# Kernel tuning notes

Measured on AMD Instinct MI355X. Metric: run time of the kernel, lower is better.

The kernel has to match this reference:

```python
import jax, jax.numpy as jnp
import numpy as np

IOU_THRESHOLD = 0.5
CLASS_CONF_THRESHOLD = 0.01
MAX_OUTPUT = 100  # tf.image.non_max_suppression max_output_size


def _nms_indices(boxes, scores, max_out, iou_thr):
    """Fixed-size greedy NMS: returns (idxs[max_out], valid[max_out])."""
    x1, y1, x2, y2 = boxes[:, 0], boxes[:, 1], boxes[:, 2], boxes[:, 3]
    areas = (x2 - x1) * (y2 - y1)

    def body(sc, _):
        i = jnp.argmax(sc)
        valid = sc[i] > 0.0  # score_threshold = 0.0 in tf call
        xx1 = jnp.maximum(x1[i], x1)
        yy1 = jnp.maximum(y1[i], y1)
        xx2 = jnp.minimum(x2[i], x2)
        yy2 = jnp.minimum(y2[i], y2)
        inter = jnp.maximum(xx2 - xx1, 0.0) * jnp.maximum(yy2 - yy1, 0.0)
        union = areas[i] + areas - inter
        iou = jnp.where(union > 0.0, inter / union, 0.0)
        # suppress overlapping boxes (self included, iou=1) only if pick valid
        sc_new = jnp.where((iou > iou_thr) & valid, -1.0, sc)
        return sc_new, (i, valid)

    _, (idxs, valids) = jax.lax.scan(body, scores, None, length=max_out)
    return idxs, valids


def _decode(x, anchors):
    B, H, W, A, C = x.shape  # B == 1
    gw = jnp.float32(W)
    # grid offsets: (col, row) per cell, matching cell_x / transposed cell_y
    cx = jnp.broadcast_to(jnp.arange(W, dtype=jnp.float32).reshape(1, 1, W, 1, 1), (1, H, W, 1, 1))
    cy = jnp.broadcast_to(jnp.arange(H, dtype=jnp.float32).reshape(1, H, 1, 1, 1), (1, H, W, 1, 1))
    grid = jnp.concatenate([cx, cy], axis=-1)  # (1,H,W,1,2)

    xy = (jax.nn.sigmoid(x[..., 0:2]) + grid) / gw                      # (B,H,W,A,2)
    wh = jnp.exp(x[..., 2:4]) * anchors.reshape(1, 1, 1, A, 2) / gw     # (B,H,W,A,2)
    boxes = jnp.concatenate([xy - wh / 2.0, xy + wh / 2.0], axis=-1)    # (B,H,W,A,4)

    conf = jax.nn.sigmoid(x[..., 4:5])                                  # (B,H,W,A,1)
    cls_prob = jax.nn.softmax(x[..., 5:], axis=-1)                      # (B,H,W,A,C-5)
    class_confidence = conf * cls_prob
    masked = jnp.where(class_confidence > CLASS_CONF_THRESHOLD, class_confidence, 0.0)
    classes = jnp.argmax(masked, axis=-1).astype(jnp.int32)             # (B,H,W,A)
    confm = jnp.max(masked, axis=-1)                                    # (B,H,W,A)

    N = H * W * A
    return boxes.reshape(N, 4), confm.reshape(N), classes.reshape(N)


def reference(x, anchors):
    boxes, scores, classes = _decode(x, anchors)
    idxs, valids = _nms_indices(jax.lax.stop_gradient(boxes),
                                jax.lax.stop_gradient(scores),
                                MAX_OUTPUT, IOU_THRESHOLD)
    sel_conf = jnp.where(valids, scores[idxs], 0.0)
    sel_boxes = jnp.where(valids[:, None], boxes[idxs], 0.0)
    sel_classes = jnp.where(valids, classes[idxs], -1)
    return sel_conf, sel_boxes, sel_classes


def setup_inputs() -> dict:
    key = jax.random.key(0)
    k1, k2 = jax.random.split(key)
    x = jax.random.normal(k1, (1, 256, 256, 5, 85), dtype=jnp.float32)
    # anchor priors in grid units (positive widths/heights)
    anchors = jax.random.uniform(k2, (5, 2), dtype=jnp.float32) * 4.0 + 0.5
    return {"x": x, "anchors": anchors}
```

## Files before the change

### kernel.cpp

```cpp
#include <hip/hip_runtime.h>
#include <hip/hip_bf16.h>

#define NROW 327680
#define NCLS 80
#define K_TARGET 1024u
#define CAP 2048u
#define MAX_OUT 100
#define NBIN 864
#define BIN0 0x3C23
#define HIST_BLOCKS 80

#define WS_SCORES 0
#define WS_PART   1310720
#define WS_CNT    1587200
#define WS_KEYS   1587264

typedef float f4v __attribute__((ext_vector_type(4)));
typedef f4v f4u __attribute__((aligned(4)));

__global__ __launch_bounds__(256, 1) void decode_score(
    const float* __restrict__ x, float* __restrict__ scores) {
  const int r = blockIdx.x * 256 + threadIdx.x;
  const float* rp = x + (size_t)r * 85;

  float conf_l = rp[4];
  float cl[80];
  #pragma unroll
  for (int c = 0; c < 20; ++c) {
    f4v t4 = *(const f4u*)(rp + 5 + 4 * c);
    cl[4*c+0] = t4.x; cl[4*c+1] = t4.y; cl[4*c+2] = t4.z; cl[4*c+3] = t4.w;
  }

  float m = cl[0];
  #pragma unroll
  for (int c = 1; c < NCLS; ++c) { float l = cl[c]; if (l > m) m = l; }
  float s = 0.f;
  #pragma unroll
  for (int c = 0; c < NCLS; ++c) s += expf(cl[c] - m);
  float conf = 1.f / (1.f + expf(-conf_l));
  float best = conf * (1.f / s);
  scores[r] = (best > 0.01f) ? best : 0.f;
}

__global__ __launch_bounds__(1024) void hist_kernel(
    const float* __restrict__ scores, unsigned* __restrict__ part) {
  __shared__ unsigned h[NBIN];
  const int t = threadIdx.x;
  if (t < NBIN) h[t] = 0;
  __syncthreads();

  float4 s4 = ((const float4*)scores)[blockIdx.x * 1024 + t];
  float sv[4] = {s4.x, s4.y, s4.z, s4.w};
  #pragma unroll
  for (int k = 0; k < 4; ++k) {
    float s = sv[k];
    if (s > 0.f) {
      int idx = (int)(__float_as_uint(s) >> 16) - BIN0;
      if (idx > NBIN - 1) idx = NBIN - 1;
      atomicAdd(&h[idx], 1u);
    }
  }
  __syncthreads();
  if (t < NBIN) part[blockIdx.x * NBIN + t] = h[t];
}

__global__ __launch_bounds__(1024) void thresh_kernel(
    const unsigned* __restrict__ part, unsigned* __restrict__ cnt) {
  __shared__ unsigned bufA[1024], bufB[1024];
  const int t = threadIdx.x;

  unsigned colsum = 0;
  if (t < NBIN) {
    unsigned a0 = 0, a1 = 0, a2 = 0, a3 = 0;
    #pragma unroll
    for (int b = 0; b < HIST_BLOCKS; b += 4) {
      a0 += part[(b + 0) * NBIN + t];
      a1 += part[(b + 1) * NBIN + t];
      a2 += part[(b + 2) * NBIN + t];
      a3 += part[(b + 3) * NBIN + t];
    }
    colsum = a0 + a1 + a2 + a3;
  }
  bufA[t] = colsum;
  __syncthreads();

  unsigned* src = bufA; unsigned* dst = bufB;
  for (int d = 1; d < 1024; d <<= 1) {
    unsigned val = src[t] + ((t + d < 1024) ? src[t + d] : 0u);
    dst[t] = val;
    __syncthreads();
    unsigned* tmp = src; src = dst; dst = tmp;
  }
  if (src[t] >= K_TARGET && (t == 1023 || src[t + 1] < K_TARGET)) {
    unsigned T = (unsigned)t;
    if (src[t] > CAP) T += 1;
    cnt[1] = T;
  }
  if (t == 0) {
    if (src[0] < K_TARGET) cnt[1] = 0;
    cnt[0] = 0;
  }
}

__global__ __launch_bounds__(256) void compact_kernel(
    const float* __restrict__ scores, unsigned* __restrict__ cnt,
    unsigned long long* __restrict__ keys) {
  __shared__ unsigned blocal, bbase;
  const int t = threadIdx.x;
  if (t == 0) blocal = 0;
  __syncthreads();

  const unsigned T = cnt[1];
  const int gi = blockIdx.x * 256 + t;
  float4 s4 = ((const float4*)scores)[gi];
  float sv[4] = {s4.x, s4.y, s4.z, s4.w};
  unsigned long long lk[4]; int nl = 0;
  #pragma unroll
  for (int k = 0; k < 4; ++k) {
    float s = sv[k];
    if (s <= 0.f) continue;
    unsigned bits = __float_as_uint(s);
    int idx = (int)(bits >> 16) - BIN0;
    if (idx > NBIN - 1) idx = NBIN - 1;
    if ((unsigned)idx < T) continue;
    unsigned r = (unsigned)(gi * 4 + k);
    lk[nl++] = ((unsigned long long)bits << 32) |
               (unsigned long long)(0xFFFFFFFFu - r);
  }
  unsigned lpos = nl ? atomicAdd(&blocal, (unsigned)nl) : 0u;
  __syncthreads();
  if (t == 0 && blocal) bbase = atomicAdd(&cnt[0], blocal);
  __syncthreads();
  if (nl) {
    unsigned base = bbase + lpos;
    for (int i = 0; i < nl; ++i)
      if (base + i < CAP) keys[base + i] = lk[i];
  }
}

__global__ __launch_bounds__(1024) void final_kernel(
    const float* __restrict__ x, const float* __restrict__ anchors,
    const unsigned* __restrict__ cnt, const unsigned long long* __restrict__ keys,
    float* __restrict__ out) {
  __shared__ unsigned long long sk[CAP];
  __shared__ float4 cbox[CAP];
  __shared__ float4 kbox[MAX_OUT];
  __shared__ float  kscore[MAX_OUT];
  __shared__ int    krow[MAX_OUT];
  __shared__ int    kcls[MAX_OUT];
  __shared__ int    knum;
  const int t = threadIdx.x;
  if (t == 0) knum = 0;

  unsigned n = cnt[0]; if (n > CAP) n = CAP;
  unsigned npow2 = 2; while (npow2 < n) npow2 <<= 1;
  for (unsigned i = t; i < npow2; i += 1024) sk[i] = (i < n) ? keys[i] : 0ull;
  __syncthreads();

  for (unsigned k = 2; k <= npow2; k <<= 1) {
    for (unsigned j = k >> 1; j > 0; j >>= 1) {
      for (unsigned p = t; p < (npow2 >> 1); p += 1024) {
        unsigned i = ((p & ~(j - 1u)) << 1) | (p & (j - 1u));
        unsigned ixj = i | j;
        unsigned long long a = sk[i], b = sk[ixj];
        bool desc = ((i & k) == 0);
        if (desc ? (a < b) : (a > b)) { sk[i] = b; sk[ixj] = a; }
      }
      __syncthreads();
    }
  }

  for (unsigned i = t; i < n; i += 1024) {
    unsigned r = 0xFFFFFFFFu - (unsigned)(sk[i] & 0xFFFFFFFFull);
    const float* rp = x + (size_t)r * 85;
    float tx = rp[0], ty = rp[1], tw = rp[2], th = rp[3];
    const int a  = (int)(r % 5u);
    const int hw = (int)(r / 5u);
    const float wf = (float)(hw & 255);
    const float hf = (float)(hw >> 8);
    float sx = 1.f / (1.f + expf(-tx));
    float sy = 1.f / (1.f + expf(-ty));
    float xc = (sx + wf) / 256.f;
    float yc = (sy + hf) / 256.f;
    float bw = expf(tw) * anchors[2*a]     / 256.f;
    float bh = expf(th) * anchors[2*a + 1] / 256.f;
    float hwd = bw / 2.f, hhd = bh / 2.f;
    cbox[i] = make_float4(xc - hwd, yc - hhd, xc + hwd, yc + hhd);
  }
  __syncthreads();

  if (t < 64) {
    int nk = 0;
    float ax1=0,ay1=0,ax2=0,ay2=0,aar=0;
    float bx1=0,by1=0,bx2=0,by2=0,bar=0;
    unsigned long long key = (n > 0) ? sk[0] : 0ull;
    float4 bb = (n > 0) ? cbox[0] : make_float4(0,0,0,0);
    for (unsigned cc = 0; cc < n && nk < MAX_OUT; ++cc) {
      unsigned long long key_n = (cc + 1 < n) ? sk[cc + 1] : 0ull;
      float4 bb_n = (cc + 1 < n) ? cbox[cc + 1] : make_float4(0,0,0,0);
      unsigned sbits = (unsigned)(key >> 32);
      if (sbits == 0u) break;
      float area = (bb.z - bb.x) * (bb.w - bb.y);
      bool s0 = false, s1 = false;
      if (t < nk) {
        float xx1 = fmaxf(ax1, bb.x), yy1 = fmaxf(ay1, bb.y);
        float xx2 = fminf(ax2, bb.z), yy2 = fminf(ay2, bb.w);
        float inter = fmaxf(xx2 - xx1, 0.f) * fmaxf(yy2 - yy1, 0.f);
        float uni = aar + area - inter;
        s0 = (uni > 0.f) && (inter / uni > 0.5f);
      }
      if (t + 64 < nk) {
        float xx1 = fmaxf(bx1, bb.x), yy1 = fmaxf(by1, bb.y);
        float xx2 = fminf(bx2, bb.z), yy2 = fminf(by2, bb.w);
        float inter = fmaxf(xx2 - xx1, 0.f) * fmaxf(yy2 - yy1, 0.f);
        float uni = bar + area - inter;
        s1 = (uni > 0.f) && (inter / uni > 0.5f);
      }
      if (!__any(s0 || s1)) {
        if (t == nk)      { ax1=bb.x; ay1=bb.y; ax2=bb.z; ay2=bb.w; aar=area; }
        if (t == nk - 64) { bx1=bb.x; by1=bb.y; bx2=bb.z; by2=bb.w; bar=area; }
        if (t == 0) {
          unsigned r = 0xFFFFFFFFu - (unsigned)(key & 0xFFFFFFFFull);
          kbox[nk] = bb; kscore[nk] = __uint_as_float(sbits); krow[nk] = (int)r;
        }
        ++nk;
      }
      key = key_n; bb = bb_n;
    }
    if (t == 0) knum = nk;
  }
  __syncthreads();

  {
    const int wv = t >> 6, lane = t & 63;
    for (int kidx = wv; kidx < knum; kidx += 16) {
      const float* rp = x + (size_t)krow[kidx] * 85;
      float l0 = rp[5 + lane];
      unsigned b0 = __float_as_uint(l0);
      b0 = (b0 & 0x80000000u) ? ~b0 : (b0 | 0x80000000u);
      unsigned long long kv =
          ((unsigned long long)b0 << 32) | (unsigned long long)(0xFFFFFFFFu - lane);
      if (lane < 16) {
        float l1 = rp[5 + 64 + lane];
        unsigned b1 = __float_as_uint(l1);
        b1 = (b1 & 0x80000000u) ? ~b1 : (b1 | 0x80000000u);
        unsigned long long kv1 =
            ((unsigned long long)b1 << 32) |
            (unsigned long long)(0xFFFFFFFFu - (64 + lane));
        if (kv1 > kv) kv = kv1;
      }
      #pragma unroll
      for (int d = 32; d >= 1; d >>= 1) {
        unsigned long long o = __shfl_xor((long long)kv, d, 64);
        if (o > kv) kv = o;
      }
      if (lane == 0)
        kcls[kidx] = (int)(0xFFFFFFFFu - (unsigned)(kv & 0xFFFFFFFFull));
    }
  }
  __syncthreads();

  if (t < MAX_OUT) {
    float conf = 0.f; float4 bb = make_float4(0.f, 0.f, 0.f, 0.f); float cf = -1.f;
    if (t < knum) { conf = kscore[t]; bb = kbox[t]; cf = (float)kcls[t]; }
    out[t] = conf;
    ((float4*)(out + 100))[t] = bb;
    out[500 + t] = cf;
  }
}

extern "C" void kernel_launch(void* const* d_in, const int* in_sizes, int n_in,
                              void* d_out, int out_size, void* d_ws, size_t ws_size,
                              hipStream_t stream) {
  const float* x       = (const float*)d_in[0];
  const float* anchors = (const float*)d_in[1];
  float* out = (float*)d_out;
  char* ws = (char*)d_ws;

  float*              scores = (float*)(ws + WS_SCORES);
  unsigned*           part   = (unsigned*)(ws + WS_PART);
  unsigned*           cnt    = (unsigned*)(ws + WS_CNT);
  unsigned long long* keys   = (unsigned long long*)(ws + WS_KEYS);

  hipLaunchKernelGGL(decode_score, dim3(NROW / 256), dim3(256),
                     0, stream, x, scores);
  hipLaunchKernelGGL(hist_kernel, dim3(HIST_BLOCKS), dim3(1024),
                     0, stream, scores, part);
  hipLaunchKernelGGL(thresh_kernel, dim3(1), dim3(1024), 0, stream, part, cnt);
  hipLaunchKernelGGL(compact_kernel, dim3(NROW / 1024), dim3(256),
                     0, stream, scores, cnt, keys);
  hipLaunchKernelGGL(final_kernel, dim3(1), dim3(1024), 0, stream,
                     x, anchors, cnt, keys, out);
}
```

Measured before the change: 237.8 us.

## Replace single-block bitonic sort and serial NMS with rank sort and IoU bitmask

The single-block bitonic sort is replaced by a multi-block rank-counting sort that also decodes candidate boxes. A new kernel precomputes a full pairwise IoU suppression bitmask matrix across many blocks. The greedy NMS loop then only ORs bitmask rows, with the first rows cached in LDS and later rows prefetched. This moves serial sort and IoU work off one workgroup, at the cost of two extra launches and the O(n^2) adjacency computation and its global writes.

```diff
diff --git a/kernel.cpp b/kernel.cpp
--- a/kernel.cpp
+++ b/kernel.cpp
@@ -5,18 +5,25 @@
 #define NCLS 80
 #define K_TARGET 1024u
 #define CAP 2048u
+#define MAXN 2048
 #define MAX_OUT 100
 #define NBIN 864
 #define BIN0 0x3C23
 #define HIST_BLOCKS 80
+#define ADJW 32
+#define ADJC_ROWS 128
 
 #define WS_SCORES 0
 #define WS_PART   1310720
 #define WS_CNT    1587200
 #define WS_KEYS   1587264
+#define WS_SORT   1603648
+#define WS_CBOX   1620032
+#define WS_ADJ    1652800
 
 typedef float f4v __attribute__((ext_vector_type(4)));
 typedef f4v f4u __attribute__((aligned(4)));
+typedef unsigned long long ull;
 
 __global__ __launch_bounds__(256, 1) void decode_score(
     const float* __restrict__ x, float* __restrict__ scores) {
@@ -104,7 +111,7 @@
 
 __global__ __launch_bounds__(256) void compact_kernel(
     const float* __restrict__ scores, unsigned* __restrict__ cnt,
-    unsigned long long* __restrict__ keys) {
+    ull* __restrict__ keys) {
   __shared__ unsigned blocal, bbase;
   const int t = threadIdx.x;
   if (t == 0) blocal = 0;
@@ -114,7 +121,7 @@
   const int gi = blockIdx.x * 256 + t;
   float4 s4 = ((const float4*)scores)[gi];
   float sv[4] = {s4.x, s4.y, s4.z, s4.w};
-  unsigned long long lk[4]; int nl = 0;
+  ull lk[4]; int nl = 0;
   #pragma unroll
   for (int k = 0; k < 4; ++k) {
     float s = sv[k];
@@ -124,8 +131,7 @@
     if (idx > NBIN - 1) idx = NBIN - 1;
     if ((unsigned)idx < T) continue;
     unsigned r = (unsigned)(gi * 4 + k);
-    lk[nl++] = ((unsigned long long)bits << 32) |
-               (unsigned long long)(0xFFFFFFFFu - r);
+    lk[nl++] = ((ull)bits << 32) | (ull)(0xFFFFFFFFu - r);
   }
   unsigned lpos = nl ? atomicAdd(&blocal, (unsigned)nl) : 0u;
   __syncthreads();
@@ -138,120 +144,141 @@
   }
 }
 
+__global__ __launch_bounds__(64) void rank_kernel(
+    const float* __restrict__ x, const float* __restrict__ anchors,
+    const unsigned* __restrict__ cnt, const ull* __restrict__ keys,
+    ull* __restrict__ sorted, float4* __restrict__ cboxg) {
+  __shared__ ull lk[MAXN];
+  unsigned n = cnt[0]; if (n > CAP) n = CAP;
+  const int t = threadIdx.x;
+  for (unsigned i = t; i < n; i += 64) lk[i] = keys[i];
+  __syncthreads();
+
+  const unsigned i = blockIdx.x * 64 + t;
+  if (i >= n) return;
+  const ull ki = lk[i];
+  unsigned rank = 0;
+  #pragma unroll 4
+  for (unsigned j = 0; j < n; ++j) rank += (lk[j] > ki) ? 1u : 0u;
+
+  sorted[rank] = ki;
+
+  unsigned r = 0xFFFFFFFFu - (unsigned)(ki & 0xFFFFFFFFull);
+  const float* rp = x + (size_t)r * 85;
+  float tx = rp[0], ty = rp[1], tw = rp[2], th = rp[3];
+  const int a  = (int)(r % 5u);
+  const int hw = (int)(r / 5u);
+  const float wf = (float)(hw & 255);
+  const float hf = (float)(hw >> 8);
+  float sx = 1.f / (1.f + expf(-tx));
+  float sy = 1.f / (1.f + expf(-ty));
+  float xc = (sx + wf) / 256.f;
+  float yc = (sy + hf) / 256.f;
+  float bw = expf(tw) * anchors[2*a]     / 256.f;
+  float bh = expf(th) * anchors[2*a + 1] / 256.f;
+  float hwd = bw / 2.f, hhd = bh / 2.f;
+  cboxg[rank] = make_float4(xc - hwd, yc - hhd, xc + hwd, yc + hhd);
+}
+
+__global__ __launch_bounds__(256) void adj_kernel(
+    const unsigned* __restrict__ cnt, const float4* __restrict__ cboxg,
+    ull* __restrict__ adj) {
+  unsigned n = cnt[0]; if (n > CAP) n = CAP;
+  const unsigned i = blockIdx.x;
+  if (i >= n) return;
+  const float4 bi = cboxg[i];
+  const float areai = (bi.z - bi.x) * (bi.w - bi.y);
+  const int t = threadIdx.x, wid = t >> 6, lane = t & 63;
+
+  #pragma unroll
+  for (int pass = 0; pass < 8; ++pass) {
+    unsigned j = (unsigned)(pass * 256 + t);
+    bool sup = false;
+    if (j < n) {
+      float4 bj = cboxg[j];
+      float xx1 = fmaxf(bi.x, bj.x), yy1 = fmaxf(bi.y, bj.y);
+      float xx2 = fminf(bi.z, bj.z), yy2 = fminf(bi.w, bj.w);
+      float inter = fmaxf(xx2 - xx1, 0.f) * fmaxf(yy2 - yy1, 0.f);
+      float areaj = (bj.z - bj.x) * (bj.w - bj.y);
+      float uni = areai + areaj - inter;
+      float iou = (uni > 0.f) ? (inter / uni) : 0.f;
+      sup = iou > 0.5f;
+    }
+    ull m = __ballot(sup);
+    if (lane == 0) adj[(size_t)i * ADJW + pass * 4 + wid] = m;
+  }
+}
+
 __global__ __launch_bounds__(1024) void final_kernel(
-    const float* __restrict__ x, const float* __restrict__ anchors,
-    const unsigned* __restrict__ cnt, const unsigned long long* __restrict__ keys,
-    float* __restrict__ out) {
-  __shared__ unsigned long long sk[CAP];
-  __shared__ float4 cbox[CAP];
-  __shared__ float4 kbox[MAX_OUT];
-  __shared__ float  kscore[MAX_OUT];
-  __shared__ int    krow[MAX_OUT];
-  __shared__ int    kcls[MAX_OUT];
-  __shared__ int    knum;
+    const float* __restrict__ x, const unsigned* __restrict__ cnt,
+    const ull* __restrict__ sorted, const float4* __restrict__ cboxg,
+    const ull* __restrict__ adjg, float* __restrict__ out) {
+  __shared__ ull sk[MAXN];
+  __shared__ ull adjc[ADJC_ROWS * ADJW];
+  __shared__ int keptcc[MAX_OUT];
+  __shared__ int kcls[MAX_OUT];
+  __shared__ int knum;
   const int t = threadIdx.x;
   if (t == 0) knum = 0;
 
   unsigned n = cnt[0]; if (n > CAP) n = CAP;
-  unsigned npow2 = 2; while (npow2 < n) npow2 <<= 1;
-  for (unsigned i = t; i < npow2; i += 1024) sk[i] = (i < n) ? keys[i] : 0ull;
-  __syncthreads();
-
-  for (unsigned k = 2; k <= npow2; k <<= 1) {
-    for (unsigned j = k >> 1; j > 0; j >>= 1) {
-      for (unsigned p = t; p < (npow2 >> 1); p += 1024) {
-        unsigned i = ((p & ~(j - 1u)) << 1) | (p & (j - 1u));
-        unsigned ixj = i | j;
-        unsigned long long a = sk[i], b = sk[ixj];
-        bool desc = ((i & k) == 0);
-        if (desc ? (a < b) : (a > b)) { sk[i] = b; sk[ixj] = a; }
+  for (unsigned i = t; i < n; i += 1024) sk[i] = sorted[i];
+  const unsigned ncache = (n < ADJC_ROWS ? n : ADJC_ROWS) * ADJW;
+  for (unsigned i = t; i < ncache; i += 1024) adjc[i] = adjg[i];
+  __syncthreads();
+
+  if (t < 64) {
+    const int lane = t;
+    ull mask = 0ull;
+    int nk = 0;
+    ull rA = 0ull, rB = 0ull;
+    if (lane < ADJW) {
+      if (n > 0) rA = adjc[0 * ADJW + lane];
+      if (n > 1) rB = (1 < ADJC_ROWS) ? adjc[1 * ADJW + lane]
+                                      : adjg[1 * ADJW + lane];
+    }
+    for (unsigned cc = 0; cc < n; ++cc) {
+      ull rC = 0ull;
+      unsigned pcc = cc + 2;
+      if (lane < ADJW && pcc < n)
+        rC = (pcc < ADJC_ROWS) ? adjc[pcc * ADJW + lane]
+                               : adjg[(size_t)pcc * ADJW + lane];
+      const int w = (int)(cc >> 6);
+      ull mw = (ull)__shfl((long long)mask, w, 64);
+      bool sup = (mw >> (cc & 63u)) & 1ull;
+      if (!sup) {
+        mask |= rA;
+        if (lane == 0) keptcc[nk] = (int)cc;
+        ++nk;
+        if (nk == MAX_OUT) break;
       }
-      __syncthreads();
-    }
-  }
-
-  for (unsigned i = t; i < n; i += 1024) {
-    unsigned r = 0xFFFFFFFFu - (unsigned)(sk[i] & 0xFFFFFFFFull);
-    const float* rp = x + (size_t)r * 85;
-    float tx = rp[0], ty = rp[1], tw = rp[2], th = rp[3];
-    const int a  = (int)(r % 5u);
-    const int hw = (int)(r / 5u);
-    const float wf = (float)(hw & 255);
-    const float hf = (float)(hw >> 8);
-    float sx = 1.f / (1.f + expf(-tx));
-    float sy = 1.f / (1.f + expf(-ty));
-    float xc = (sx + wf) / 256.f;
-    float yc = (sy + hf) / 256.f;
-    float bw = expf(tw) * anchors[2*a]     / 256.f;
-    float bh = expf(th) * anchors[2*a + 1] / 256.f;
-    float hwd = bw / 2.f, hhd = bh / 2.f;
-    cbox[i] = make_float4(xc - hwd, yc - hhd, xc + hwd, yc + hhd);
-  }
-  __syncthreads();
-
-  if (t < 64) {
-    int nk = 0;
-    float ax1=0,ay1=0,ax2=0,ay2=0,aar=0;
-    float bx1=0,by1=0,bx2=0,by2=0,bar=0;
-    unsigned long long key = (n > 0) ? sk[0] : 0ull;
-    float4 bb = (n > 0) ? cbox[0] : make_float4(0,0,0,0);
-    for (unsigned cc = 0; cc < n && nk < MAX_OUT; ++cc) {
-      unsigned long long key_n = (cc + 1 < n) ? sk[cc + 1] : 0ull;
-      float4 bb_n = (cc + 1 < n) ? cbox[cc + 1] : make_float4(0,0,0,0);
-      unsigned sbits = (unsigned)(key >> 32);
-      if (sbits == 0u) break;
-      float area = (bb.z - bb.x) * (bb.w - bb.y);
-      bool s0 = false, s1 = false;
-      if (t < nk) {
-        float xx1 = fmaxf(ax1, bb.x), yy1 = fmaxf(ay1, bb.y);
-        float xx2 = fminf(ax2, bb.z), yy2 = fminf(ay2, bb.w);
-        float inter = fmaxf(xx2 - xx1, 0.f) * fmaxf(yy2 - yy1, 0.f);
-        float uni = aar + area - inter;
-        s0 = (uni > 0.f) && (inter / uni > 0.5f);
-      }
-      if (t + 64 < nk) {
-        float xx1 = fmaxf(bx1, bb.x), yy1 = fmaxf(by1, bb.y);
-        float xx2 = fminf(bx2, bb.z), yy2 = fminf(by2, bb.w);
-        float inter = fmaxf(xx2 - xx1, 0.f) * fmaxf(yy2 - yy1, 0.f);
-        float uni = bar + area - inter;
-        s1 = (uni > 0.f) && (inter / uni > 0.5f);
-      }
-      if (!__any(s0 || s1)) {
-        if (t == nk)      { ax1=bb.x; ay1=bb.y; ax2=bb.z; ay2=bb.w; aar=area; }
-        if (t == nk - 64) { bx1=bb.x; by1=bb.y; bx2=bb.z; by2=bb.w; bar=area; }
-        if (t == 0) {
-          unsigned r = 0xFFFFFFFFu - (unsigned)(key & 0xFFFFFFFFull);
-          kbox[nk] = bb; kscore[nk] = __uint_as_float(sbits); krow[nk] = (int)r;
-        }
-        ++nk;
-      }
-      key = key_n; bb = bb_n;
-    }
-    if (t == 0) knum = nk;
-  }
-  __syncthreads();
+      rA = rB; rB = rC;
+    }
+    if (lane == 0) knum = nk;
+  }
+  __syncthreads();
+  const int kn = knum;
 
   {
     const int wv = t >> 6, lane = t & 63;
-    for (int kidx = wv; kidx < knum; kidx += 16) {
-      const float* rp = x + (size_t)krow[kidx] * 85;
+    for (int kidx = wv; kidx < kn; kidx += 16) {
+      ull key = sk[keptcc[kidx]];
+      unsigned r = 0xFFFFFFFFu - (unsigned)(key & 0xFFFFFFFFull);
+      const float* rp = x + (size_t)r * 85;
       float l0 = rp[5 + lane];
       unsigned b0 = __float_as_uint(l0);
       b0 = (b0 & 0x80000000u) ? ~b0 : (b0 | 0x80000000u);
-      unsigned long long kv =
-          ((unsigned long long)b0 << 32) | (unsigned long long)(0xFFFFFFFFu - lane);
+      ull kv = ((ull)b0 << 32) | (ull)(0xFFFFFFFFu - lane);
       if (lane < 16) {
         float l1 = rp[5 + 64 + lane];
         unsigned b1 = __float_as_uint(l1);
         b1 = (b1 & 0x80000000u) ? ~b1 : (b1 | 0x80000000u);
-        unsigned long long kv1 =
-            ((unsigned long long)b1 << 32) |
-            (unsigned long long)(0xFFFFFFFFu - (64 + lane));
+        ull kv1 = ((ull)b1 << 32) | (ull)(0xFFFFFFFFu - (64 + lane));
         if (kv1 > kv) kv = kv1;
       }
       #pragma unroll
       for (int d = 32; d >= 1; d >>= 1) {
-        unsigned long long o = __shfl_xor((long long)kv, d, 64);
+        ull o = (ull)__shfl_xor((long long)kv, d, 64);
         if (o > kv) kv = o;
       }
       if (lane == 0)
@@ -262,7 +289,13 @@
 
   if (t < MAX_OUT) {
     float conf = 0.f; float4 bb = make_float4(0.f, 0.f, 0.f, 0.f); float cf = -1.f;
-    if (t < knum) { conf = kscore[t]; bb = kbox[t]; cf = (float)kcls[t]; }
+    if (t < kn) {
+      int cc = keptcc[t];
+      ull key = sk[cc];
+      conf = __uint_as_float((unsigned)(key >> 32));
+      bb = cboxg[cc];
+      cf = (float)kcls[t];
+    }
     out[t] = conf;
     ((float4*)(out + 100))[t] = bb;
     out[500 + t] = cf;
@@ -277,10 +310,13 @@
   float* out = (float*)d_out;
   char* ws = (char*)d_ws;
 
-  float*              scores = (float*)(ws + WS_SCORES);
-  unsigned*           part   = (unsigned*)(ws + WS_PART);
-  unsigned*           cnt    = (unsigned*)(ws + WS_CNT);
-  unsigned long long* keys   = (unsigned long long*)(ws + WS_KEYS);
+  float*    scores = (float*)(ws + WS_SCORES);
+  unsigned* part   = (unsigned*)(ws + WS_PART);
+  unsigned* cnt    = (unsigned*)(ws + WS_CNT);
+  ull*      keys   = (ull*)(ws + WS_KEYS);
+  ull*      sorted = (ull*)(ws + WS_SORT);
+  float4*   cboxg  = (float4*)(ws + WS_CBOX);
+  ull*      adj    = (ull*)(ws + WS_ADJ);
 
   hipLaunchKernelGGL(decode_score, dim3(NROW / 256), dim3(256),
                      0, stream, x, scores);
@@ -289,6 +325,10 @@
   hipLaunchKernelGGL(thresh_kernel, dim3(1), dim3(1024), 0, stream, part, cnt);
   hipLaunchKernelGGL(compact_kernel, dim3(NROW / 1024), dim3(256),
                      0, stream, scores, cnt, keys);
+  hipLaunchKernelGGL(rank_kernel, dim3(MAXN / 64), dim3(64),
+                     0, stream, x, anchors, cnt, keys, sorted, cboxg);
+  hipLaunchKernelGGL(adj_kernel, dim3(MAXN), dim3(256),
+                     0, stream, cnt, cboxg, adj);
   hipLaunchKernelGGL(final_kernel, dim3(1), dim3(1024), 0, stream,
-                     x, anchors, cnt, keys, out);
-}
+                     x, cnt, sorted, cboxg, adj, out);
+}
```

After: 236.1 us. Within noise of the previous version (-0.7%).
